# Optimization experiments

Measured on AMD Instinct MI355X. Metric: run time of the kernel, lower is better.

Reference implementation:

```python
import jax, jax.numpy as jnp
import numpy as np

D_MODEL = 1024
N_HEADS = 16
HEAD_DIM = D_MODEL // N_HEADS
SCALE = HEAD_DIM ** (-0.5)
D_GRAPH = 8
B, N = 4, 1024
NEG_INF = -1.0e9


def setup_inputs() -> dict:
    key = jax.random.key(0)
    ks = jax.random.split(key, 8)
    std = (2.0 / (5.0 * D_MODEL)) ** 0.5
    q = jax.random.normal(ks[0], (B, N, D_MODEL), dtype=jnp.float32)
    k = jax.random.normal(ks[1], (B, N, D_MODEL), dtype=jnp.float32)
    v = jax.random.normal(ks[2], (B, N, D_MODEL), dtype=jnp.float32)
    mask = jax.random.randint(ks[3], (B, N), 0, 2).astype(bool)
    graphormer_dists = jax.random.uniform(ks[4], (B, N, N, D_GRAPH), dtype=jnp.float32)
    weights = std * jax.random.normal(ks[5], (4 * D_MODEL, D_MODEL), dtype=jnp.float32)
    biases = jnp.zeros((4 * D_MODEL,), dtype=jnp.float32)
    w_graph = std * jax.random.normal(ks[6], (N_HEADS, D_GRAPH), dtype=jnp.float32)
    return {"q": q, "k": k, "v": v, "mask": mask,
            "graphormer_dists": graphormer_dists,
            "weights": weights, "biases": biases, "w_graph": w_graph}


def _proj(x, weights, biases, start, end):
    # F.linear with a slice of the fused [4*d_model, d_model] weight
    return x @ weights[start:end].T + biases[start:end]


def _split_heads(x):
    b, n, _ = x.shape
    return x.reshape(b, n, N_HEADS, HEAD_DIM).transpose(0, 2, 1, 3)  # bhnd


def reference(q, k, v, mask, graphormer_dists, weights, biases, w_graph):
    b, n, _ = q.shape
    qh = _split_heads(_proj(q, weights, biases, 0, D_MODEL))
    kh = _split_heads(_proj(k, weights, biases, D_MODEL, 2 * D_MODEL))
    vh = _split_heads(_proj(v, weights, biases, 2 * D_MODEL, 3 * D_MODEL))
    # dot-product scores, scaled
    att = jnp.einsum('bhnd,bhmd->bhnm', qh, kh) * SCALE
    # graphormer bias: Linear(d_graph -> n_heads), then permute to bhnm
    att = att + jnp.einsum('bnmp,hp->bhnm', graphormer_dists, w_graph)
    # mask fills along the QUERY dim (mask[:,None,:,None]), as in the source
    att = jnp.where(mask[:, None, :, None], NEG_INF, att)
    att = jax.nn.softmax(att, axis=-1)
    # dropout p=0.0 (eval): identity
    out = jnp.einsum('bhnm,bhmd->bhnd', att, vh)
    out = out.transpose(0, 2, 1, 3).reshape(b, n, D_MODEL)
    out = _proj(out, weights, biases, 3 * D_MODEL, 4 * D_MODEL)
    return out, att
```

## Files before the change

### kernel.cpp

```cpp
#include <hip/hip_runtime.h>
#include <hip/hip_bf16.h>

#define SEQ      1024
#define BATCH    4
#define NHEADS   16
#define HDIM     64
#define DMODEL   1024
#define DGRAPH   8
#define QK_SCALE 0.125f
#define PCONST   0.0009765625f

typedef __attribute__((ext_vector_type(8))) short bf16x8;
typedef __attribute__((ext_vector_type(4))) short bf16x4;
typedef __attribute__((ext_vector_type(4))) float f32x4;

__device__ __forceinline__ void split_bf16(float x, short& hi, short& lo) {
    unsigned u = __float_as_uint(x);
    hi = (short)(u >> 16);
    float hf = __uint_as_float(u & 0xffff0000u);
    lo = (short)(__float_as_uint(x - hf) >> 16);
}

__global__ __launch_bounds__(256) void prep_split(
    const float* __restrict__ X, short* __restrict__ Hi, short* __restrict__ Lo)
{
    const int idx = blockIdx.x * 256 + threadIdx.x;
    const float* p = X + (size_t)idx * 8;
    float4 u0 = *(const float4*)p;
    float4 u1 = *(const float4*)(p + 4);
    float v[8] = {u0.x, u0.y, u0.z, u0.w, u1.x, u1.y, u1.z, u1.w};
    bf16x8 hv, lv;
#pragma unroll
    for (int j = 0; j < 8; ++j) {
        short h, s; split_bf16(v[j], h, s);
        hv[j] = h; lv[j] = s;
    }
    *(bf16x8*)(Hi + (size_t)idx * 8) = hv;
    *(bf16x8*)(Lo + (size_t)idx * 8) = lv;
}

template<int INMODE, int OUTMODE>
__global__ __launch_bounds__(256) void proj_mfma(
    const float* __restrict__ X,
    const short* __restrict__ Xhi, const short* __restrict__ Xlo,
    const short* __restrict__ Whi, const short* __restrict__ Wlo,
    const float* __restrict__ bias,
    float* __restrict__ Yf,
    short* __restrict__ Yhi,
    short* __restrict__ Ylo,
    float scale)
{
    constexpr int LDK = 40;
    __shared__ short Ah[128 * LDK];
    __shared__ short Al[128 * LDK];
    __shared__ short Bh[64 * LDK];
    __shared__ short Bl[64 * LDK];

    const int t   = threadIdx.x;
    const int w   = t >> 6;
    const int l   = t & 63;
    const int l15 = l & 15;
    const int lk  = (l >> 4) * 8;
    const int m0  = blockIdx.y * 128;
    const int c0  = blockIdx.x * 64;
    const int wr  = (w >> 1) * 64;
    const int wc  = (w & 1) * 32;

    const int srow = t >> 2;
    const int skg  = t & 3;

    f32x4 acc[4][2];
#pragma unroll
    for (int i = 0; i < 4; ++i)
#pragma unroll
        for (int j = 0; j < 2; ++j) acc[i][j] = f32x4{0.f, 0.f, 0.f, 0.f};

    float  xa[2][8];
    bf16x8 xh[2], xl[2];
    bf16x8 wh, wl;

    if constexpr (INMODE == 0) {
#pragma unroll
        for (int i = 0; i < 2; ++i) {
            const float* p = X + (size_t)(m0 + srow + i * 64) * DMODEL + skg * 8;
            float4 u0 = *(const float4*)p;
            float4 u1 = *(const float4*)(p + 4);
            xa[i][0] = u0.x; xa[i][1] = u0.y; xa[i][2] = u0.z; xa[i][3] = u0.w;
            xa[i][4] = u1.x; xa[i][5] = u1.y; xa[i][6] = u1.z; xa[i][7] = u1.w;
        }
    } else {
#pragma unroll
        for (int i = 0; i < 2; ++i) {
            const size_t off = (size_t)(m0 + srow + i * 64) * DMODEL + skg * 8;
            xh[i] = *(const bf16x8*)(Xhi + off);
            xl[i] = *(const bf16x8*)(Xlo + off);
        }
    }
    {
        const size_t off = (size_t)(c0 + srow) * DMODEL + skg * 8;
        wh = *(const bf16x8*)(Whi + off);
        wl = *(const bf16x8*)(Wlo + off);
    }

    for (int kt = 0; kt < 32; ++kt) {
        if constexpr (INMODE == 0) {
#pragma unroll
            for (int i = 0; i < 2; ++i) {
                bf16x8 hv, lv;
#pragma unroll
                for (int j = 0; j < 8; ++j) {
                    short h, s; split_bf16(xa[i][j], h, s);
                    hv[j] = h; lv[j] = s;
                }
                *(bf16x8*)(Ah + (srow + i * 64) * LDK + skg * 8) = hv;
                *(bf16x8*)(Al + (srow + i * 64) * LDK + skg * 8) = lv;
            }
        } else {
#pragma unroll
            for (int i = 0; i < 2; ++i) {
                *(bf16x8*)(Ah + (srow + i * 64) * LDK + skg * 8) = xh[i];
                *(bf16x8*)(Al + (srow + i * 64) * LDK + skg * 8) = xl[i];
            }
        }
        *(bf16x8*)(Bh + srow * LDK + skg * 8) = wh;
        *(bf16x8*)(Bl + srow * LDK + skg * 8) = wl;
        __syncthreads();

        if (kt + 1 < 32) {
            const int k0 = (kt + 1) * 32;
            if constexpr (INMODE == 0) {
#pragma unroll
                for (int i = 0; i < 2; ++i) {
                    const float* p = X + (size_t)(m0 + srow + i * 64) * DMODEL + k0 + skg * 8;
                    float4 u0 = *(const float4*)p;
                    float4 u1 = *(const float4*)(p + 4);
                    xa[i][0] = u0.x; xa[i][1] = u0.y; xa[i][2] = u0.z; xa[i][3] = u0.w;
                    xa[i][4] = u1.x; xa[i][5] = u1.y; xa[i][6] = u1.z; xa[i][7] = u1.w;
                }
            } else {
#pragma unroll
                for (int i = 0; i < 2; ++i) {
                    const size_t off = (size_t)(m0 + srow + i * 64) * DMODEL + k0 + skg * 8;
                    xh[i] = *(const bf16x8*)(Xhi + off);
                    xl[i] = *(const bf16x8*)(Xlo + off);
                }
            }
            const size_t off = (size_t)(c0 + srow) * DMODEL + k0 + skg * 8;
            wh = *(const bf16x8*)(Whi + off);
            wl = *(const bf16x8*)(Wlo + off);
        }

        bf16x8 ah[4], alo[4], bh[2], blo[2];
#pragma unroll
        for (int fm = 0; fm < 4; ++fm) {
            const int off = (wr + fm * 16 + l15) * LDK + lk;
            ah[fm]  = *(const bf16x8*)(Ah + off);
            alo[fm] = *(const bf16x8*)(Al + off);
        }
#pragma unroll
        for (int fn = 0; fn < 2; ++fn) {
            const int off = (wc + fn * 16 + l15) * LDK + lk;
            bh[fn]  = *(const bf16x8*)(Bh + off);
            blo[fn] = *(const bf16x8*)(Bl + off);
        }
#pragma unroll
        for (int fm = 0; fm < 4; ++fm)
#pragma unroll
            for (int fn = 0; fn < 2; ++fn) {
                acc[fm][fn] = __builtin_amdgcn_mfma_f32_16x16x32_bf16(
                    ah[fm], bh[fn], acc[fm][fn], 0, 0, 0);
                acc[fm][fn] = __builtin_amdgcn_mfma_f32_16x16x32_bf16(
                    ah[fm], blo[fn], acc[fm][fn], 0, 0, 0);
                acc[fm][fn] = __builtin_amdgcn_mfma_f32_16x16x32_bf16(
                    alo[fm], bh[fn], acc[fm][fn], 0, 0, 0);
            }
        __syncthreads();
    }

#pragma unroll
    for (int fm = 0; fm < 4; ++fm)
#pragma unroll
        for (int fn = 0; fn < 2; ++fn) {
            const int c = c0 + wc + fn * 16 + l15;
            const float bb = bias[c];
#pragma unroll
            for (int r = 0; r < 4; ++r) {
                const int m = m0 + wr + fm * 16 + (l >> 4) * 4 + r;
                const float v = (acc[fm][fn][r] + bb) * scale;
                if constexpr (OUTMODE == 0) {
                    Yf[(size_t)m * DMODEL + c] = v;
                } else {
                    const int b_ = m >> 10, n = m & 1023;
                    const int h = c >> 6, d = c & 63;
                    short hi, lo; split_bf16(v, hi, lo);
                    if constexpr (OUTMODE == 2) {
                        const size_t idx =
                            ((size_t)((b_ * NHEADS + h) * SEQ + n)) * HDIM + d;
                        Yhi[idx] = hi; Ylo[idx] = lo;
                    } else {
                        const size_t idx =
                            ((size_t)((b_ * NHEADS + h) * HDIM + d)) * SEQ + n;
                        Yhi[idx] = hi; Ylo[idx] = lo;
                    }
                }
            }
        }
}

__global__ __launch_bounds__(256) void graph_bias_kernel(
    const float* __restrict__ dists,
    const float* __restrict__ wg,
    const int* __restrict__ mask,
    float* __restrict__ attL,
    float* __restrict__ rowSum)
{
    const int n = blockIdx.x & 1023;
    const int b = blockIdx.x >> 10;
    const int t = threadIdx.x;
    if (t < NHEADS)
        rowSum[(size_t)(b * NHEADS + t) * SEQ + n] = 0.f;
    if (mask[b * SEQ + n]) return;

    __shared__ float wgs[NHEADS * DGRAPH];
    if (t < NHEADS * DGRAPH) wgs[t] = wg[t];
    __syncthreads();

    const int m = t * 4;
    const float* dp = dists + (((size_t)(b * SEQ + n)) * SEQ + m) * DGRAPH;
    float d[4][8];
#pragma unroll
    for (int i = 0; i < 8; ++i) {
        float4 v = *reinterpret_cast<const float4*>(dp + i * 4);
        d[i >> 1][(i & 1) * 4 + 0] = v.x; d[i >> 1][(i & 1) * 4 + 1] = v.y;
        d[i >> 1][(i & 1) * 4 + 2] = v.z; d[i >> 1][(i & 1) * 4 + 3] = v.w;
    }
#pragma unroll
    for (int h = 0; h < NHEADS; ++h) {
        float ov[4];
#pragma unroll
        for (int jm = 0; jm < 4; ++jm) {
            float s = 0.f;
#pragma unroll
            for (int p = 0; p < DGRAPH; ++p)
                s = fmaf(d[jm][p], wgs[h * DGRAPH + p], s);
            ov[jm] = s;
        }
        float4 o; o.x = ov[0]; o.y = ov[1]; o.z = ov[2]; o.w = ov[3];
        *reinterpret_cast<float4*>(
            attL + (((size_t)((b * NHEADS + h) * SEQ + n)) * SEQ + m)) = o;
    }
}

__global__ __launch_bounds__(256) void qk_mfma(
    const short* __restrict__ Qhi, const short* __restrict__ Qlo,
    const short* __restrict__ Khi, const short* __restrict__ Klo,
    const int* __restrict__ mask,
    float* __restrict__ attL,
    float* __restrict__ rowSum)
{
    constexpr int LDK = 72;
    __shared__ short sQh[128 * LDK];
    __shared__ short sQl[128 * LDK];
    __shared__ short sKh[128 * LDK];
    __shared__ short sKl[128 * LDK];
    __shared__ int maskS[128];

    const int t   = threadIdx.x;
    const int w   = t >> 6;
    const int l   = t & 63;
    const int l15 = l & 15;
    const int lk  = (l >> 4) * 8;
    const int m0  = blockIdx.x * 128;
    const int n0  = blockIdx.y * 128;
    const int bh  = blockIdx.z;
    const int b   = bh >> 4;

    if (t < 128) maskS[t] = mask[b * SEQ + n0 + t];

#pragma unroll
    for (int it = 0; it < 4; ++it) {
        const int f   = t + it * 256;
        const int row = f >> 3;
        const int c8  = f & 7;
        const size_t gq = ((size_t)bh * SEQ + n0 + row) * HDIM + c8 * 8;
        const size_t gk = ((size_t)bh * SEQ + m0 + row) * HDIM + c8 * 8;
        const int lo = row * LDK + c8 * 8;
        *(bf16x8*)(sQh + lo) = *(const bf16x8*)(Qhi + gq);
        *(bf16x8*)(sQl + lo) = *(const bf16x8*)(Qlo + gq);
        *(bf16x8*)(sKh + lo) = *(const bf16x8*)(Khi + gk);
        *(bf16x8*)(sKl + lo) = *(const bf16x8*)(Klo + gk);
    }
    __syncthreads();

    const int nr = (w >> 1) * 64;
    const int mc = (w & 1) * 64;

    f32x4 acc[4][4];
    {
        const float* bb = attL + ((size_t)bh * SEQ + n0 + nr + (l >> 4) * 4) * SEQ
                          + m0 + mc + l15;
#pragma unroll
        for (int fm = 0; fm < 4; ++fm)
#pragma unroll
            for (int r = 0; r < 4; ++r) {
                const int nloc = nr + fm * 16 + (l >> 4) * 4 + r;
                const bool mk = maskS[nloc] != 0;
#pragma unroll
                for (int fn = 0; fn < 4; ++fn)
                    acc[fm][fn][r] =
                        mk ? 0.f : bb[(size_t)(fm * 16 + r) * SEQ + fn * 16];
            }
    }

#pragma unroll
    for (int ks = 0; ks < 2; ++ks) {
        bf16x8 ah[4], alo[4], bhv[4], blo[4];
#pragma unroll
        for (int fm = 0; fm < 4; ++fm) {
            const int off = (nr + fm * 16 + l15) * LDK + ks * 32 + lk;
            ah[fm]  = *(const bf16x8*)(sQh + off);
            alo[fm] = *(const bf16x8*)(sQl + off);
        }
#pragma unroll
        for (int fn = 0; fn < 4; ++fn) {
            const int off = (mc + fn * 16 + l15) * LDK + ks * 32 + lk;
            bhv[fn] = *(const bf16x8*)(sKh + off);
            blo[fn] = *(const bf16x8*)(sKl + off);
        }
#pragma unroll
        for (int fm = 0; fm < 4; ++fm)
#pragma unroll
            for (int fn = 0; fn < 4; ++fn) {
                acc[fm][fn] = __builtin_amdgcn_mfma_f32_16x16x32_bf16(
                    ah[fm], bhv[fn], acc[fm][fn], 0, 0, 0);
                acc[fm][fn] = __builtin_amdgcn_mfma_f32_16x16x32_bf16(
                    ah[fm], blo[fn], acc[fm][fn], 0, 0, 0);
                acc[fm][fn] = __builtin_amdgcn_mfma_f32_16x16x32_bf16(
                    alo[fm], bhv[fn], acc[fm][fn], 0, 0, 0);
            }
    }

#pragma unroll
    for (int fm = 0; fm < 4; ++fm)
#pragma unroll
        for (int r = 0; r < 4; ++r) {
            const int nloc = nr + fm * 16 + (l >> 4) * 4 + r;
            const bool msk = maskS[nloc] != 0;
            float* rowp = attL + ((size_t)bh * SEQ + n0 + nloc) * SEQ + m0 + mc + l15;
            float s = 0.f;
#pragma unroll
            for (int fn = 0; fn < 4; ++fn) {
                const float e = __expf(acc[fm][fn][r]);
                s += e;
                if (!msk) rowp[fn * 16] = e;
            }
            s += __shfl_xor(s, 1); s += __shfl_xor(s, 2);
            s += __shfl_xor(s, 4); s += __shfl_xor(s, 8);
            if (!msk && l15 == 0)
                atomicAdd(rowSum + (size_t)bh * SEQ + n0 + nloc, s);
        }
}

__global__ __launch_bounds__(256) void pv_mfma(
    float* __restrict__ attL,
    const short* __restrict__ VThi,
    const short* __restrict__ VTlo,
    const int* __restrict__ mask,
    const float* __restrict__ rowSum,
    short* __restrict__ AOhi,
    short* __restrict__ AOlo)
{
    constexpr int LDP = 72;
    __shared__ short pHi[128 * LDP];
    __shared__ short pLo[128 * LDP];
    __shared__ short sVh[64 * LDP];
    __shared__ short sVl[64 * LDP];
    __shared__ float rowInv[128];
    __shared__ int   maskS[128];

    const int t   = threadIdx.x;
    const int w   = t >> 6;
    const int l   = t & 63;
    const int l15 = l & 15;
    const int lk  = (l >> 4) * 8;
    const int n0  = blockIdx.x * 128;
    const int h   = blockIdx.y;
    const int b   = blockIdx.z;
    const int bh  = b * NHEADS + h;
    float* Lbase = attL + ((size_t)bh * SEQ + n0) * SEQ;

    if (t < 128) {
        const int mk = mask[b * SEQ + n0 + t];
        maskS[t] = mk;
        rowInv[t] = mk ? 0.f : 1.0f / rowSum[(size_t)bh * SEQ + n0 + t];
    }
    __syncthreads();

    const int nr = (w >> 1) * 64;
    const int dc = (w & 1) * 32;

    f32x4 acc[4][2];
#pragma unroll
    for (int i = 0; i < 4; ++i)
#pragma unroll
        for (int j = 0; j < 2; ++j) acc[i][j] = f32x4{0.f, 0.f, 0.f, 0.f};

    float4 sreg[8];
#pragma unroll
    for (int i = 0; i < 8; ++i) sreg[i] = make_float4(0.f, 0.f, 0.f, 0.f);
#pragma unroll
    for (int i = 0; i < 8; ++i) {
        const int f4 = t + i * 256;
        const int row = f4 >> 4, mq = f4 & 15;
        if (!maskS[row])
            sreg[i] = *reinterpret_cast<const float4*>(
                Lbase + (size_t)row * SEQ + mq * 4);
    }

    for (int mc = 0; mc < 16; ++mc) {
#pragma unroll
        for (int i = 0; i < 8; ++i) {
            const int f4 = t + i * 256;
            const int row = f4 >> 4, mq = f4 & 15;
            float4 p4;
            if (maskS[row]) {
                p4.x = PCONST; p4.y = PCONST; p4.z = PCONST; p4.w = PCONST;
            } else {
                const float iv = rowInv[row];
                p4.x = sreg[i].x * iv; p4.y = sreg[i].y * iv;
                p4.z = sreg[i].z * iv; p4.w = sreg[i].w * iv;
            }
            *reinterpret_cast<float4*>(
                Lbase + (size_t)row * SEQ + mc * 64 + mq * 4) = p4;
            bf16x4 hv, lv;
            short h0, s0, h1, s1, h2, s2, h3, s3;
            split_bf16(p4.x, h0, s0); split_bf16(p4.y, h1, s1);
            split_bf16(p4.z, h2, s2); split_bf16(p4.w, h3, s3);
            hv[0] = h0; hv[1] = h1; hv[2] = h2; hv[3] = h3;
            lv[0] = s0; lv[1] = s1; lv[2] = s2; lv[3] = s3;
            *(bf16x4*)(pHi + row * LDP + mq * 4) = hv;
            *(bf16x4*)(pLo + row * LDP + mq * 4) = lv;
        }
#pragma unroll
        for (int i = 0; i < 2; ++i) {
            const int f = t + i * 256;
            const int d = f >> 3, m8 = f & 7;
            const size_t src = ((size_t)bh * HDIM + d) * SEQ + mc * 64 + m8 * 8;
            *(bf16x8*)(sVh + d * LDP + m8 * 8) = *(const bf16x8*)(VThi + src);
            *(bf16x8*)(sVl + d * LDP + m8 * 8) = *(const bf16x8*)(VTlo + src);
        }
        __syncthreads();

        if (mc + 1 < 16) {
#pragma unroll
            for (int i = 0; i < 8; ++i) {
                const int f4 = t + i * 256;
                const int row = f4 >> 4, mq = f4 & 15;
                if (!maskS[row])
                    sreg[i] = *reinterpret_cast<const float4*>(
                        Lbase + (size_t)row * SEQ + (mc + 1) * 64 + mq * 4);
            }
        }

#pragma unroll
        for (int ks = 0; ks < 2; ++ks) {
            bf16x8 ah[4], alo[4], bhv[2], blo[2];
#pragma unroll
            for (int fm = 0; fm < 4; ++fm) {
                const int off = (nr + fm * 16 + l15) * LDP + ks * 32 + lk;
                ah[fm]  = *(const bf16x8*)(pHi + off);
                alo[fm] = *(const bf16x8*)(pLo + off);
            }
#pragma unroll
            for (int fn = 0; fn < 2; ++fn) {
                const int off = (dc + fn * 16 + l15) * LDP + ks * 32 + lk;
                bhv[fn] = *(const bf16x8*)(sVh + off);
                blo[fn] = *(const bf16x8*)(sVl + off);
            }
#pragma unroll
            for (int fm = 0; fm < 4; ++fm)
#pragma unroll
                for (int fn = 0; fn < 2; ++fn) {
                    acc[fm][fn] = __builtin_amdgcn_mfma_f32_16x16x32_bf16(
                        ah[fm], bhv[fn], acc[fm][fn], 0, 0, 0);
                    acc[fm][fn] = __builtin_amdgcn_mfma_f32_16x16x32_bf16(
                        ah[fm], blo[fn], acc[fm][fn], 0, 0, 0);
                    acc[fm][fn] = __builtin_amdgcn_mfma_f32_16x16x32_bf16(
                        alo[fm], bhv[fn], acc[fm][fn], 0, 0, 0);
                }
        }
        __syncthreads();
    }

#pragma unroll
    for (int fm = 0; fm < 4; ++fm)
#pragma unroll
        for (int fn = 0; fn < 2; ++fn) {
            const int dd = dc + fn * 16 + l15;
#pragma unroll
            for (int r = 0; r < 4; ++r) {
                const int n = n0 + nr + fm * 16 + (l >> 4) * 4 + r;
                const size_t idx =
                    ((size_t)(b * SEQ + n)) * DMODEL + h * HDIM + dd;
                short hi, lo; split_bf16(acc[fm][fn][r], hi, lo);
                AOhi[idx] = hi; AOlo[idx] = lo;
            }
        }
}

extern "C" void kernel_launch(void* const* d_in, const int* in_sizes, int n_in,
                              void* d_out, int out_size, void* d_ws, size_t ws_size,
                              hipStream_t stream) {
    const float* q       = (const float*)d_in[0];
    const float* k       = (const float*)d_in[1];
    const float* v       = (const float*)d_in[2];
    const int*   mask    = (const int*)d_in[3];
    const float* dists   = (const float*)d_in[4];
    const float* weights = (const float*)d_in[5];
    const float* biases  = (const float*)d_in[6];
    const float* wg      = (const float*)d_in[7];

    float* out  = (float*)d_out;
    float* attL = out + (size_t)BATCH * SEQ * DMODEL;

    const size_t HSZ = (size_t)BATCH * NHEADS * SEQ * HDIM;
    const size_t WSZ = (size_t)4 * DMODEL * DMODEL;
    short* Qhi  = (short*)d_ws;
    short* Qlo  = Qhi + HSZ;
    short* Khi  = Qlo + HSZ;
    short* Klo  = Khi + HSZ;
    short* VThi = Klo + HSZ;
    short* VTlo = VThi + HSZ;
    short* Whi  = VTlo + HSZ;
    short* Wlo  = Whi + WSZ;
    short* AOhi = Qhi;
    short* AOlo = Qlo;
    float* rowSum = out;

    const size_t DD = (size_t)DMODEL * DMODEL;

    prep_split<<<(int)(WSZ / 8 / 256), 256, 0, stream>>>(weights, Whi, Wlo);

    graph_bias_kernel<<<BATCH * SEQ, 256, 0, stream>>>(dists, wg, mask, attL, rowSum);

    dim3 gProj(DMODEL / 64, (BATCH * SEQ) / 128);
    proj_mfma<0, 2><<<gProj, 256, 0, stream>>>(q, nullptr, nullptr,
        Whi, Wlo, biases, nullptr, Qhi, Qlo, QK_SCALE);
    proj_mfma<0, 2><<<gProj, 256, 0, stream>>>(k, nullptr, nullptr,
        Whi + DD, Wlo + DD, biases + DMODEL, nullptr, Khi, Klo, 1.0f);
    proj_mfma<0, 3><<<gProj, 256, 0, stream>>>(v, nullptr, nullptr,
        Whi + 2 * DD, Wlo + 2 * DD, biases + 2 * DMODEL, nullptr, VThi, VTlo, 1.0f);

    dim3 gQK(SEQ / 128, SEQ / 128, BATCH * NHEADS);
    qk_mfma<<<gQK, 256, 0, stream>>>(Qhi, Qlo, Khi, Klo, mask, attL, rowSum);

    dim3 gPV(SEQ / 128, NHEADS, BATCH);
    pv_mfma<<<gPV, 256, 0, stream>>>(attL, VThi, VTlo, mask, rowSum, AOhi, AOlo);

    proj_mfma<1, 0><<<gProj, 256, 0, stream>>>(nullptr, AOhi, AOlo,
        Whi + 3 * DD, Wlo + 3 * DD, biases + 3 * DMODEL, out, nullptr, nullptr, 1.0f);
}
```

Before: 438.4 us.

## Store graph bias and exp scores as bf16 in att buffer, loop QK over keys

The graph-bias kernel now writes bf16 values into the first half of each fp32 attention row, and the QK kernel writes bf16 exp values into the second half. This halves intermediate traffic before pv_mfma writes the final fp32 probabilities. The QK kernel now loops over all key tiles per block, so it accumulates row sums in registers and LDS and writes them directly instead of zero-initialising and using global atomics. The cost is bf16 rounding of the bias and exp values, which may loosen accuracy, and a smaller grid for the QK kernel.

```diff
diff --git a/kernel.cpp b/kernel.cpp
--- a/kernel.cpp
+++ b/kernel.cpp
@@ -13,12 +13,23 @@
 typedef __attribute__((ext_vector_type(8))) short bf16x8;
 typedef __attribute__((ext_vector_type(4))) short bf16x4;
 typedef __attribute__((ext_vector_type(4))) float f32x4;
+typedef __attribute__((ext_vector_type(8))) unsigned short u16x8;
+typedef __attribute__((ext_vector_type(4))) unsigned short u16x4;
 
 __device__ __forceinline__ void split_bf16(float x, short& hi, short& lo) {
     unsigned u = __float_as_uint(x);
     hi = (short)(u >> 16);
     float hf = __uint_as_float(u & 0xffff0000u);
     lo = (short)(__float_as_uint(x - hf) >> 16);
+}
+
+__device__ __forceinline__ unsigned short f2bf(float x) {
+    unsigned u = __float_as_uint(x);
+    u += 0x7fffu + ((u >> 16) & 1u);
+    return (unsigned short)(u >> 16);
+}
+__device__ __forceinline__ float bf2f(unsigned short v) {
+    return __uint_as_float((unsigned)v << 16);
 }
 
 __global__ __launch_bounds__(256) void prep_split(
@@ -211,17 +222,14 @@
     const float* __restrict__ dists,
     const float* __restrict__ wg,
     const int* __restrict__ mask,
-    float* __restrict__ attL,
-    float* __restrict__ rowSum)
+    float* __restrict__ attL)
 {
     const int n = blockIdx.x & 1023;
     const int b = blockIdx.x >> 10;
+    if (mask[b * SEQ + n]) return;
+
+    __shared__ float wgs[NHEADS * DGRAPH];
     const int t = threadIdx.x;
-    if (t < NHEADS)
-        rowSum[(size_t)(b * NHEADS + t) * SEQ + n] = 0.f;
-    if (mask[b * SEQ + n]) return;
-
-    __shared__ float wgs[NHEADS * DGRAPH];
     if (t < NHEADS * DGRAPH) wgs[t] = wg[t];
     __syncthreads();
 
@@ -236,18 +244,18 @@
     }
 #pragma unroll
     for (int h = 0; h < NHEADS; ++h) {
-        float ov[4];
+        u16x4 o;
 #pragma unroll
         for (int jm = 0; jm < 4; ++jm) {
             float s = 0.f;
 #pragma unroll
             for (int p = 0; p < DGRAPH; ++p)
                 s = fmaf(d[jm][p], wgs[h * DGRAPH + p], s);
-            ov[jm] = s;
-        }
-        float4 o; o.x = ov[0]; o.y = ov[1]; o.z = ov[2]; o.w = ov[3];
-        *reinterpret_cast<float4*>(
-            attL + (((size_t)((b * NHEADS + h) * SEQ + n)) * SEQ + m)) = o;
+            o[jm] = f2bf(s);
+        }
+        unsigned short* rowp = (unsigned short*)
+            (attL + (((size_t)((b * NHEADS + h) * SEQ + n)) * SEQ));
+        *(u16x4*)(rowp + m) = o;
     }
 }
 
@@ -263,19 +271,19 @@
     __shared__ short sQl[128 * LDK];
     __shared__ short sKh[128 * LDK];
     __shared__ short sKl[128 * LDK];
-    __shared__ int maskS[128];
+    __shared__ float rsLDS[128];
+    __shared__ int   maskS[128];
 
     const int t   = threadIdx.x;
     const int w   = t >> 6;
     const int l   = t & 63;
     const int l15 = l & 15;
     const int lk  = (l >> 4) * 8;
-    const int m0  = blockIdx.x * 128;
-    const int n0  = blockIdx.y * 128;
-    const int bh  = blockIdx.z;
+    const int n0  = blockIdx.x * 128;
+    const int bh  = blockIdx.y;
     const int b   = bh >> 4;
 
-    if (t < 128) maskS[t] = mask[b * SEQ + n0 + t];
+    if (t < 128) { maskS[t] = mask[b * SEQ + n0 + t]; rsLDS[t] = 0.f; }
 
 #pragma unroll
     for (int it = 0; it < 4; ++it) {
@@ -283,82 +291,114 @@
         const int row = f >> 3;
         const int c8  = f & 7;
         const size_t gq = ((size_t)bh * SEQ + n0 + row) * HDIM + c8 * 8;
-        const size_t gk = ((size_t)bh * SEQ + m0 + row) * HDIM + c8 * 8;
         const int lo = row * LDK + c8 * 8;
         *(bf16x8*)(sQh + lo) = *(const bf16x8*)(Qhi + gq);
         *(bf16x8*)(sQl + lo) = *(const bf16x8*)(Qlo + gq);
-        *(bf16x8*)(sKh + lo) = *(const bf16x8*)(Khi + gk);
-        *(bf16x8*)(sKl + lo) = *(const bf16x8*)(Klo + gk);
-    }
-    __syncthreads();
-
-    const int nr = (w >> 1) * 64;
-    const int mc = (w & 1) * 64;
-
-    f32x4 acc[4][4];
-    {
-        const float* bb = attL + ((size_t)bh * SEQ + n0 + nr + (l >> 4) * 4) * SEQ
-                          + m0 + mc + l15;
+    }
+
+    const int nr  = (w >> 1) * 64;
+    const int mcw = (w & 1) * 64;
+
+    unsigned short* attU = (unsigned short*)attL;
+    const size_t rowStride = 2 * SEQ;
+    const size_t blkBase = ((size_t)bh * SEQ + n0) * rowStride;
+
+    float rsum[4][4];
+#pragma unroll
+    for (int i = 0; i < 4; ++i)
+#pragma unroll
+        for (int j = 0; j < 4; ++j) rsum[i][j] = 0.f;
+
+    for (int mt = 0; mt < 8; ++mt) {
+        const int m0 = mt * 128;
+#pragma unroll
+        for (int it = 0; it < 4; ++it) {
+            const int f   = t + it * 256;
+            const int row = f >> 3;
+            const int c8  = f & 7;
+            const size_t gk = ((size_t)bh * SEQ + m0 + row) * HDIM + c8 * 8;
+            const int lo = row * LDK + c8 * 8;
+            *(bf16x8*)(sKh + lo) = *(const bf16x8*)(Khi + gk);
+            *(bf16x8*)(sKl + lo) = *(const bf16x8*)(Klo + gk);
+        }
+        __syncthreads();
+
+        f32x4 acc[4][4];
 #pragma unroll
         for (int fm = 0; fm < 4; ++fm)
 #pragma unroll
             for (int r = 0; r < 4; ++r) {
                 const int nloc = nr + fm * 16 + (l >> 4) * 4 + r;
                 const bool mk = maskS[nloc] != 0;
+                const unsigned short* bp =
+                    attU + blkBase + (size_t)nloc * rowStride + m0 + mcw + l15;
 #pragma unroll
                 for (int fn = 0; fn < 4; ++fn)
-                    acc[fm][fn][r] =
-                        mk ? 0.f : bb[(size_t)(fm * 16 + r) * SEQ + fn * 16];
-            }
-    }
-
-#pragma unroll
-    for (int ks = 0; ks < 2; ++ks) {
-        bf16x8 ah[4], alo[4], bhv[4], blo[4];
-#pragma unroll
-        for (int fm = 0; fm < 4; ++fm) {
-            const int off = (nr + fm * 16 + l15) * LDK + ks * 32 + lk;
-            ah[fm]  = *(const bf16x8*)(sQh + off);
-            alo[fm] = *(const bf16x8*)(sQl + off);
-        }
-#pragma unroll
-        for (int fn = 0; fn < 4; ++fn) {
-            const int off = (mc + fn * 16 + l15) * LDK + ks * 32 + lk;
-            bhv[fn] = *(const bf16x8*)(sKh + off);
-            blo[fn] = *(const bf16x8*)(sKl + off);
-        }
+                    acc[fm][fn][r] = mk ? 0.f : bf2f(bp[fn * 16]);
+            }
+
+#pragma unroll
+        for (int ks = 0; ks < 2; ++ks) {
+            bf16x8 ah[4], alo[4], bhv[4], blo[4];
+#pragma unroll
+            for (int fm = 0; fm < 4; ++fm) {
+                const int off = (nr + fm * 16 + l15) * LDK + ks * 32 + lk;
+                ah[fm]  = *(const bf16x8*)(sQh + off);
+                alo[fm] = *(const bf16x8*)(sQl + off);
+            }
+#pragma unroll
+            for (int fn = 0; fn < 4; ++fn) {
+                const int off = (mcw + fn * 16 + l15) * LDK + ks * 32 + lk;
+                bhv[fn] = *(const bf16x8*)(sKh + off);
+                blo[fn] = *(const bf16x8*)(sKl + off);
+            }
+#pragma unroll
+            for (int fm = 0; fm < 4; ++fm)
+#pragma unroll
+                for (int fn = 0; fn < 4; ++fn) {
+                    acc[fm][fn] = __builtin_amdgcn_mfma_f32_16x16x32_bf16(
+                        ah[fm], bhv[fn], acc[fm][fn], 0, 0, 0);
+                    acc[fm][fn] = __builtin_amdgcn_mfma_f32_16x16x32_bf16(
+                        ah[fm], blo[fn], acc[fm][fn], 0, 0, 0);
+                    acc[fm][fn] = __builtin_amdgcn_mfma_f32_16x16x32_bf16(
+                        alo[fm], bhv[fn], acc[fm][fn], 0, 0, 0);
+                }
+        }
+
 #pragma unroll
         for (int fm = 0; fm < 4; ++fm)
 #pragma unroll
-            for (int fn = 0; fn < 4; ++fn) {
-                acc[fm][fn] = __builtin_amdgcn_mfma_f32_16x16x32_bf16(
-                    ah[fm], bhv[fn], acc[fm][fn], 0, 0, 0);
-                acc[fm][fn] = __builtin_amdgcn_mfma_f32_16x16x32_bf16(
-                    ah[fm], blo[fn], acc[fm][fn], 0, 0, 0);
-                acc[fm][fn] = __builtin_amdgcn_mfma_f32_16x16x32_bf16(
-                    alo[fm], bhv[fn], acc[fm][fn], 0, 0, 0);
-            }
+            for (int r = 0; r < 4; ++r) {
+                const int nloc = nr + fm * 16 + (l >> 4) * 4 + r;
+                const bool msk = maskS[nloc] != 0;
+                unsigned short* ep =
+                    attU + blkBase + (size_t)nloc * rowStride + SEQ + m0 + mcw + l15;
+#pragma unroll
+                for (int fn = 0; fn < 4; ++fn) {
+                    const float e = __expf(acc[fm][fn][r]);
+                    const unsigned short eb = f2bf(e);
+                    rsum[fm][r] += bf2f(eb);
+                    if (!msk) ep[fn * 16] = eb;
+                }
+            }
+        __syncthreads();
     }
 
 #pragma unroll
     for (int fm = 0; fm < 4; ++fm)
 #pragma unroll
         for (int r = 0; r < 4; ++r) {
-            const int nloc = nr + fm * 16 + (l >> 4) * 4 + r;
-            const bool msk = maskS[nloc] != 0;
-            float* rowp = attL + ((size_t)bh * SEQ + n0 + nloc) * SEQ + m0 + mc + l15;
-            float s = 0.f;
-#pragma unroll
-            for (int fn = 0; fn < 4; ++fn) {
-                const float e = __expf(acc[fm][fn][r]);
-                s += e;
-                if (!msk) rowp[fn * 16] = e;
-            }
+            float s = rsum[fm][r];
             s += __shfl_xor(s, 1); s += __shfl_xor(s, 2);
             s += __shfl_xor(s, 4); s += __shfl_xor(s, 8);
-            if (!msk && l15 == 0)
-                atomicAdd(rowSum + (size_t)bh * SEQ + n0 + nloc, s);
-        }
+            if (l15 == 0) {
+                const int nloc = nr + fm * 16 + (l >> 4) * 4 + r;
+                atomicAdd(&rsLDS[nloc], s);
+            }
+        }
+    __syncthreads();
+    if (t < 128 && !maskS[t])
+        rowSum[(size_t)bh * SEQ + n0 + t] = rsLDS[t];
 }
 
 __global__ __launch_bounds__(256) void pv_mfma(
@@ -388,6 +428,8 @@
     const int b   = blockIdx.z;
     const int bh  = b * NHEADS + h;
     float* Lbase = attL + ((size_t)bh * SEQ + n0) * SEQ;
+    const unsigned short* Ebase =
+        (const unsigned short*)Lbase;
 
     if (t < 128) {
         const int mk = mask[b * SEQ + n0 + t];
@@ -405,41 +447,45 @@
 #pragma unroll
         for (int j = 0; j < 2; ++j) acc[i][j] = f32x4{0.f, 0.f, 0.f, 0.f};
 
-    float4 sreg[8];
-#pragma unroll
-    for (int i = 0; i < 8; ++i) sreg[i] = make_float4(0.f, 0.f, 0.f, 0.f);
-#pragma unroll
-    for (int i = 0; i < 8; ++i) {
-        const int f4 = t + i * 256;
-        const int row = f4 >> 4, mq = f4 & 15;
+    u16x8 sreg[4];
+#pragma unroll
+    for (int i = 0; i < 4; ++i) sreg[i] = u16x8{0,0,0,0,0,0,0,0};
+#pragma unroll
+    for (int i = 0; i < 4; ++i) {
+        const int u = t + i * 256;
+        const int row = u >> 3, g = u & 7;
         if (!maskS[row])
-            sreg[i] = *reinterpret_cast<const float4*>(
-                Lbase + (size_t)row * SEQ + mq * 4);
+            sreg[i] = *(const u16x8*)(Ebase + (size_t)row * 2 * SEQ + SEQ + g * 8);
     }
 
     for (int mc = 0; mc < 16; ++mc) {
 #pragma unroll
-        for (int i = 0; i < 8; ++i) {
-            const int f4 = t + i * 256;
-            const int row = f4 >> 4, mq = f4 & 15;
-            float4 p4;
+        for (int i = 0; i < 4; ++i) {
+            const int u = t + i * 256;
+            const int row = u >> 3, g = u & 7;
+            float pv[8];
             if (maskS[row]) {
-                p4.x = PCONST; p4.y = PCONST; p4.z = PCONST; p4.w = PCONST;
+#pragma unroll
+                for (int j = 0; j < 8; ++j) pv[j] = PCONST;
             } else {
                 const float iv = rowInv[row];
-                p4.x = sreg[i].x * iv; p4.y = sreg[i].y * iv;
-                p4.z = sreg[i].z * iv; p4.w = sreg[i].w * iv;
-            }
-            *reinterpret_cast<float4*>(
-                Lbase + (size_t)row * SEQ + mc * 64 + mq * 4) = p4;
-            bf16x4 hv, lv;
-            short h0, s0, h1, s1, h2, s2, h3, s3;
-            split_bf16(p4.x, h0, s0); split_bf16(p4.y, h1, s1);
-            split_bf16(p4.z, h2, s2); split_bf16(p4.w, h3, s3);
-            hv[0] = h0; hv[1] = h1; hv[2] = h2; hv[3] = h3;
-            lv[0] = s0; lv[1] = s1; lv[2] = s2; lv[3] = s3;
-            *(bf16x4*)(pHi + row * LDP + mq * 4) = hv;
-            *(bf16x4*)(pLo + row * LDP + mq * 4) = lv;
+#pragma unroll
+                for (int j = 0; j < 8; ++j) pv[j] = bf2f(sreg[i][j]) * iv;
+            }
+            float4 o0, o1;
+            o0.x = pv[0]; o0.y = pv[1]; o0.z = pv[2]; o0.w = pv[3];
+            o1.x = pv[4]; o1.y = pv[5]; o1.z = pv[6]; o1.w = pv[7];
+            float* wp = Lbase + (size_t)row * SEQ + mc * 64 + g * 8;
+            *reinterpret_cast<float4*>(wp)     = o0;
+            *reinterpret_cast<float4*>(wp + 4) = o1;
+            bf16x8 hv, lv;
+#pragma unroll
+            for (int j = 0; j < 8; ++j) {
+                short hh, ss; split_bf16(pv[j], hh, ss);
+                hv[j] = hh; lv[j] = ss;
+            }
+            *(bf16x8*)(pHi + row * LDP + g * 8) = hv;
+            *(bf16x8*)(pLo + row * LDP + g * 8) = lv;
         }
 #pragma unroll
         for (int i = 0; i < 2; ++i) {
@@ -453,12 +499,12 @@
 
         if (mc + 1 < 16) {
 #pragma unroll
-            for (int i = 0; i < 8; ++i) {
-                const int f4 = t + i * 256;
-                const int row = f4 >> 4, mq = f4 & 15;
+            for (int i = 0; i < 4; ++i) {
+                const int u = t + i * 256;
+                const int row = u >> 3, g = u & 7;
                 if (!maskS[row])
-                    sreg[i] = *reinterpret_cast<const float4*>(
-                        Lbase + (size_t)row * SEQ + (mc + 1) * 64 + mq * 4);
+                    sreg[i] = *(const u16x8*)(
+                        Ebase + (size_t)row * 2 * SEQ + SEQ + (mc + 1) * 64 + g * 8);
             }
         }
 
@@ -541,7 +587,7 @@
 
     prep_split<<<(int)(WSZ / 8 / 256), 256, 0, stream>>>(weights, Whi, Wlo);
 
-    graph_bias_kernel<<<BATCH * SEQ, 256, 0, stream>>>(dists, wg, mask, attL, rowSum);
+    graph_bias_kernel<<<BATCH * SEQ, 256, 0, stream>>>(dists, wg, mask, attL);
 
     dim3 gProj(DMODEL / 64, (BATCH * SEQ) / 128);
     proj_mfma<0, 2><<<gProj, 256, 0, stream>>>(q, nullptr, nullptr,
@@ -551,7 +597,7 @@
     proj_mfma<0, 3><<<gProj, 256, 0, stream>>>(v, nullptr, nullptr,
         Whi + 2 * DD, Wlo + 2 * DD, biases + 2 * DMODEL, nullptr, VThi, VTlo, 1.0f);
 
-    dim3 gQK(SEQ / 128, SEQ / 128, BATCH * NHEADS);
+    dim3 gQK(SEQ / 128, BATCH * NHEADS);
     qk_mfma<<<gQK, 256, 0, stream>>>(Qhi, Qlo, Khi, Klo, mask, attL, rowSum);
 
     dim3 gPV(SEQ / 128, NHEADS, BATCH);
```

Result: slower. 546.6 us (+24.7%).
